# Kernel optimization log

Measured on AMD Instinct MI355X. Metric: run time of the kernel, lower is better.

## Reference

```python
import jax, jax.numpy as jnp
import numpy as np

NUM_IMAGE_PATCHES = 4096
HIDDEN = 1536
NUM_HEADS = 12
HEAD_DIM = HIDDEN // NUM_HEADS  # 128
MLP_HIDDEN = 4 * HIDDEN  # 6144
TXT_LEN = 256
L_X = TXT_LEN + NUM_IMAGE_PATCHES  # 4352
NUM_CONCEPTS = 20
L_C = NUM_CONCEPTS + NUM_IMAGE_PATCHES  # 4116


def setup_inputs() -> dict:
    key = jax.random.key(0)
    ks = jax.random.split(key, 10)
    B = 1
    f = lambda k, s, sc=1.0: jax.random.normal(k, s, dtype=jnp.float32) * sc
    return {
        "x": f(ks[0], (B, L_X, HIDDEN)),
        "concepts": f(ks[1], (B, NUM_CONCEPTS, HIDDEN)),
        "vec": f(ks[2], (B, HIDDEN)),
        "pe": f(ks[3], (1, 1, L_X, HEAD_DIM // 2, 2, 2)),
        "concept_pe": f(ks[4], (1, 1, L_C, HEAD_DIM // 2, 2, 2)),
        # linear1: hidden -> 3*hidden + mlp_hidden (torch Linear: y = x @ W.T + b)
        "w1": f(ks[5], (3 * HIDDEN + MLP_HIDDEN, HIDDEN), 0.02),
        "b1": jnp.zeros((3 * HIDDEN + MLP_HIDDEN,), jnp.float32),
        # linear2: hidden + mlp_hidden -> hidden
        "w2": f(ks[6], (HIDDEN, HIDDEN + MLP_HIDDEN), 0.02),
        "b2": jnp.zeros((HIDDEN,), jnp.float32),
        # QKNorm learned RMSNorm scales (per head_dim)
        "q_scale": jnp.ones((HEAD_DIM,), jnp.float32),
        "k_scale": jnp.ones((HEAD_DIM,), jnp.float32),
        # Modulation(double=False): silu(vec) -> 3*hidden (shift, scale, gate)
        "mod_w": f(ks[7], (3 * HIDDEN, HIDDEN), 0.02),
        "mod_b": jnp.zeros((3 * HIDDEN,), jnp.float32),
    }


def _layernorm(x):  # elementwise_affine=False, eps=1e-6
    mu = x.mean(-1, keepdims=True)
    var = ((x - mu) ** 2).mean(-1, keepdims=True)
    return (x - mu) * jax.lax.rsqrt(var + 1e-6)


def _rmsnorm(x, scale):  # FLUX RMSNorm with learned scale
    return x * jax.lax.rsqrt((x * x).mean(-1, keepdims=True) + 1e-6) * scale


def _apply_rope(t, pe):
    # t: [B,H,L,D]; pe: [1,1,L,D/2,2,2]
    ts = t.reshape(*t.shape[:-1], -1, 1, 2)  # [B,H,L,D/2,1,2]
    out = pe[..., 0] * ts[..., 0] + pe[..., 1] * ts[..., 1]  # [B,H,L,D/2,2]
    return out.reshape(t.shape)


def _attention(q, k, v, pe):
    q = _apply_rope(q, pe)
    k = _apply_rope(k, pe)
    scale = jnp.asarray(1.0 / np.sqrt(q.shape[-1]), q.dtype)
    logits = jnp.einsum("bhqd,bhkd->bhqk", q, k) * scale
    a = jax.nn.softmax(logits, axis=-1)
    o = jnp.einsum("bhqk,bhkd->bhqd", a, v)
    B, H, L, D = o.shape
    return o.transpose(0, 2, 1, 3).reshape(B, L, H * D)  # B L (H D)


def reference(x, concepts, vec, pe, concept_pe, w1, b1, w2, b2,
              q_scale, k_scale, mod_w, mod_b):
    H = HIDDEN
    # Modulation: lin(silu(vec))[:, None].chunk(3) -> shift, scale, gate
    m = jax.nn.silu(vec) @ mod_w.T + mod_b
    shift, scale, gate = [t[:, None, :] for t in jnp.split(m, 3, axis=-1)]

    def block(inp, pe_in):
        xm = (1.0 + scale) * _layernorm(inp) + shift
        h = xm @ w1.T + b1
        qkv, mlp = h[..., : 3 * H], h[..., 3 * H:]
        B, L = inp.shape[0], inp.shape[1]
        # 'B L (K H D) -> K B H L D'
        qkv = qkv.reshape(B, L, 3, NUM_HEADS, HEAD_DIM).transpose(2, 0, 3, 1, 4)
        q, k, v = qkv[0], qkv[1], qkv[2]
        q = _rmsnorm(q, q_scale)
        k = _rmsnorm(k, k_scale)
        attn = _attention(q, k, v, pe_in)
        return jnp.concatenate([attn, jax.nn.gelu(mlp, approximate=True)], axis=2) @ w2.T + b2

    output = block(x, pe)

    img = x[:, -NUM_IMAGE_PATCHES:]
    img_concept_x = jnp.concatenate([concepts, img], axis=1)
    output_img_concept = block(img_concept_x, concept_pe)
    concept_output = output_img_concept[:, :-NUM_IMAGE_PATCHES]

    return (x + gate * output, concepts + gate * concept_output)
```

## Files before the change

### kernel.cpp

```cpp
#include <hip/hip_runtime.h>
#include <cstdint>
#include <cstddef>

typedef float        f32x4  __attribute__((ext_vector_type(4)));
typedef __bf16       bf16x8 __attribute__((ext_vector_type(8)));
typedef unsigned int u32x4  __attribute__((ext_vector_type(4)));
typedef unsigned int u32x2  __attribute__((ext_vector_type(2)));

static constexpr int HID   = 1536;
static constexpr int NHEAD = 12;
static constexpr int HD    = 128;
static constexpr int NQKV  = 10752;
static constexpr int CATK  = 7680;
static constexpr int LX    = 4352;
static constexpr int LC2   = 4116;
static constexpr int NCON  = 20;

static constexpr float QSCL = 0.08838834764831845f * 1.4426950408889634f;

static constexpr size_t OFF_MVEC = 0;
static constexpr size_t OFF_W1B  = 18432;
static constexpr size_t OFF_W2B  = OFF_W1B  + 33030144ull;
static constexpr size_t OFF_XM1  = OFF_W2B  + 23592960ull;
static constexpr size_t OFF_QH1  = OFF_XM1;
static constexpr size_t OFF_QKV1 = OFF_XM1  + 13369344ull;
static constexpr size_t OFF_KH1  = OFF_QKV1 + 26738688ull;
static constexpr size_t OFF_VH1  = OFF_KH1  + 13369344ull;
static constexpr size_t OFF_CAT1 = OFF_VH1  + 13369344ull;
static constexpr size_t OFF_XM2  = OFF_CAT1;
static constexpr size_t OFF_QKV2 = OFF_XM2  + 196608ull;
static constexpr size_t OFF_VH2S = OFF_QKV2 + 196608ull;
static constexpr size_t OFF_QH2  = OFF_VH2S + 98304ull;
static constexpr size_t OFF_KH2  = OFF_QH2  + 196608ull;
static constexpr size_t OFF_CAT2 = OFF_KH2  + 12644352ull;

__device__ __forceinline__ void gload_lds16(const void* g, void* l)
{
  __builtin_amdgcn_global_load_lds(
      (const __attribute__((address_space(1))) unsigned int*)g,
      (__attribute__((address_space(3))) unsigned int*)l, 16, 0, 0);
}


__global__ __launch_bounds__(256) void f2b_kernel(const float* __restrict__ in,
                                                  __bf16* __restrict__ out, int n4)
{
  int i = blockIdx.x * 256 + threadIdx.x;
  if (i >= n4) return;
  f32x4 v = *((const f32x4*)in + i);
  union { __bf16 h[4]; u32x2 u; } cv;
  cv.h[0] = (__bf16)v[0]; cv.h[1] = (__bf16)v[1];
  cv.h[2] = (__bf16)v[2]; cv.h[3] = (__bf16)v[3];
  *((u32x2*)out + i) = cv.u;
}

__global__ __launch_bounds__(256) void mod_kernel(const float* __restrict__ vec,
                                                  const float* __restrict__ mod_w,
                                                  const float* __restrict__ mod_b,
                                                  float* __restrict__ m)
{
  int o = blockIdx.x * 4 + (threadIdx.x >> 6);
  int lane = threadIdx.x & 63;
  float s = 0.0f;
  for (int k = lane; k < HID; k += 64) {
    float v = vec[k];
    float sv = v / (1.0f + expf(-v));
    s += sv * mod_w[(size_t)o * HID + k];
  }
  #pragma unroll
  for (int msk = 32; msk; msk >>= 1) s += __shfl_xor(s, msk);
  if (lane == 0) m[o] = s + mod_b[o];
}

__device__ __forceinline__ float block_sum256(float v, float* red)
{
  #pragma unroll
  for (int msk = 32; msk; msk >>= 1) v += __shfl_xor(v, msk);
  int w = threadIdx.x >> 6;
  if ((threadIdx.x & 63) == 0) red[w] = v;
  __syncthreads();
  float s = red[0] + red[1] + red[2] + red[3];
  __syncthreads();
  return s;
}

__global__ __launch_bounds__(256) void ln_mod_kernel(const float* __restrict__ x,
                                                     const float* __restrict__ mvec,
                                                     __bf16* __restrict__ out)
{
  __shared__ float red[4];
  size_t row = blockIdx.x;
  const float* xr = x + row * HID;
  float v[6]; float s = 0.0f;
  #pragma unroll
  for (int i = 0; i < 6; i++) { v[i] = xr[threadIdx.x + i * 256]; s += v[i]; }
  float mu = block_sum256(s, red) * (1.0f / HID);
  float s2 = 0.0f;
  #pragma unroll
  for (int i = 0; i < 6; i++) { float d = v[i] - mu; s2 += d * d; }
  float var = block_sum256(s2, red) * (1.0f / HID);
  float rinv = rsqrtf(var + 1e-6f);
  #pragma unroll
  for (int i = 0; i < 6; i++) {
    int h = threadIdx.x + i * 256;
    float xm = (v[i] - mu) * rinv;
    xm = (1.0f + mvec[HID + h]) * xm + mvec[h];
    out[row * HID + h] = (__bf16)xm;
  }
}

template<int MODE>
__global__ __launch_bounds__(256) void gemm_bt(const __bf16* __restrict__ A,
                                               const __bf16* __restrict__ B,
                                               int M, int K,
                                               const float* __restrict__ bias,
                                               __bf16* __restrict__ qkv_out,
                                               __bf16* __restrict__ cat_out,
                                               __bf16* __restrict__ vh_out, int vkeys,
                                               const float* __restrict__ res,
                                               const float* __restrict__ gate,
                                               float* __restrict__ out)
{
  const int tid = threadIdx.x;
  const int lane = tid & 63, wave = tid >> 6;
  const int quad = lane >> 4, l16 = lane & 15;
  const int m0 = blockIdx.y * 128, n0 = blockIdx.x * 128;
  const int wm = (wave & 1) * 64, wn = (wave >> 1) * 64;

  __shared__ __bf16 As[128][64];
  __shared__ __bf16 Bs[128][64];

  const f32x4 fzero = {0.0f, 0.0f, 0.0f, 0.0f};
  f32x4 acc[4][4];
  #pragma unroll
  for (int i = 0; i < 4; i++)
    #pragma unroll
    for (int j = 0; j < 4; j++) acc[i][j] = fzero;

  const int srow = lane >> 3;
  const int scol = (lane & 7) * 8;
  const int rbase = wave * 32 + srow;
  const __bf16* Ab = A + (size_t)(m0 + rbase) * K + scol;
  const __bf16* Bb = B + (size_t)(n0 + rbase) * K + scol;

  for (int k0 = 0; k0 < K; k0 += 64) {
    __syncthreads();
    #pragma unroll
    for (int j = 0; j < 4; j++) {
      gload_lds16(Ab + (size_t)(j * 8) * K + k0, &As[wave * 32 + j * 8][0]);
      gload_lds16(Bb + (size_t)(j * 8) * K + k0, &Bs[wave * 32 + j * 8][0]);
    }
    __syncthreads();
    #pragma unroll
    for (int kk = 0; kk < 64; kk += 32) {
      bf16x8 af[4], bfr[4];
      #pragma unroll
      for (int i = 0; i < 4; i++) af[i]  = *(const bf16x8*)&As[wm + i * 16 + l16][kk + quad * 8];
      #pragma unroll
      for (int j = 0; j < 4; j++) bfr[j] = *(const bf16x8*)&Bs[wn + j * 16 + l16][kk + quad * 8];
      #pragma unroll
      for (int i = 0; i < 4; i++)
        #pragma unroll
        for (int j = 0; j < 4; j++)
          acc[i][j] = __builtin_amdgcn_mfma_f32_16x16x32_bf16(af[i], bfr[j], acc[i][j], 0, 0, 0);
    }
  }

  #pragma unroll
  for (int i = 0; i < 4; i++) {
    #pragma unroll
    for (int r = 0; r < 4; r++) {
      int gm = m0 + wm + i * 16 + quad * 4 + r;
      if (gm >= M) continue;
      #pragma unroll
      for (int j = 0; j < 4; j++) {
        int gn = n0 + wn + j * 16 + l16;
        float v = acc[i][j][r] + bias[gn];
        if constexpr (MODE == 0) {
          if (gn < 3072) {
            qkv_out[(size_t)gm * 3072 + gn] = (__bf16)v;
          } else if (gn < 4608) {
            vh_out[(size_t)(gn - 3072) * vkeys + gm] = (__bf16)v;
          } else {
            float g = 0.5f * v * (1.0f + tanhf(0.7978845608028654f * (v + 0.044715f * v * v * v)));
            cat_out[(size_t)gm * CATK + (gn - 3072)] = (__bf16)g;
          }
        } else {
          out[(size_t)gm * HID + gn] = res[(size_t)gm * HID + gn] + gate[gn] * v;
        }
      }
    }
  }
}

__global__ __launch_bounds__(256) void qk_prep(const __bf16* __restrict__ src0, int rows0,
                                               const __bf16* __restrict__ src1, int off1,
                                               int total_rows, int q_rows,
                                               const float* __restrict__ pe,
                                               const float* __restrict__ qscale,
                                               const float* __restrict__ kscale,
                                               __bf16* __restrict__ qh, int q_stride,
                                               __bf16* __restrict__ kh, int k_stride)
{
  int wid = blockIdx.x * 4 + (threadIdx.x >> 6);
  int lane = threadIdx.x & 63;
  int r = wid / NHEAD, h = wid - (wid / NHEAD) * NHEAD;
  if (r >= total_rows) return;
  const __bf16* src = (r < rows0) ? (src0 + (size_t)r * 3072)
                                  : (src1 + (size_t)(r + off1) * 3072);
  const float* pep = pe + ((size_t)r * 64 + lane) * 4;
  float e00 = pep[0], e01 = pep[1], e10 = pep[2], e11 = pep[3];

  {
    const __bf16* p = src + HID + h * HD + 2 * lane;
    float a = (float)p[0], b = (float)p[1];
    float ss = a * a + b * b;
    #pragma unroll
    for (int msk = 32; msk; msk >>= 1) ss += __shfl_xor(ss, msk);
    float rinv = rsqrtf(ss * (1.0f / HD) + 1e-6f);
    a *= rinv * kscale[2 * lane]; b *= rinv * kscale[2 * lane + 1];
    float ra = e00 * a + e01 * b, rb = e10 * a + e11 * b;
    __bf16* o = kh + ((size_t)h * k_stride + r) * HD + 2 * lane;
    o[0] = (__bf16)ra; o[1] = (__bf16)rb;
  }
  if (r < q_rows) {
    const __bf16* p = src + h * HD + 2 * lane;
    float a = (float)p[0], b = (float)p[1];
    float ss = a * a + b * b;
    #pragma unroll
    for (int msk = 32; msk; msk >>= 1) ss += __shfl_xor(ss, msk);
    float rinv = rsqrtf(ss * (1.0f / HD) + 1e-6f);
    a *= rinv * qscale[2 * lane]; b *= rinv * qscale[2 * lane + 1];
    float ra = (e00 * a + e01 * b) * QSCL, rb = (e10 * a + e11 * b) * QSCL;
    __bf16* o = qh + ((size_t)h * q_stride + r) * HD + 2 * lane;
    o[0] = (__bf16)ra; o[1] = (__bf16)rb;
  }
}

template<int GEN>
__global__ __launch_bounds__(512, 4) void attn_kernel(const __bf16* __restrict__ qh,
                                                      const __bf16* __restrict__ kh,
                                                      const __bf16* __restrict__ vA, int vA_stride,
                                                      const __bf16* __restrict__ vB, int vB_stride,
                                                      int v_boff, int v_split,
                                                      int Lq, int Lk, int q_stride, int k_stride,
                                                      int nqt,
                                                      __bf16* __restrict__ cat_out)
{
  const int tid = threadIdx.x, lane = tid & 63, wave = tid >> 6;
  const int quad = lane >> 4, l16 = lane & 15;
  const int qsub = wave >> 1, kg = wave & 1;

  int bid = blockIdx.x;
  if constexpr (GEN == 0) {
    int nb = gridDim.x;
    if ((nb & 7) == 0) {
      int per = nb >> 3;
      bid = (bid & 7) * per + (bid >> 3);
    }
  }
  const int head = bid / nqt, qt = bid - head * nqt;
  const int q0 = qt * 64 + qsub * 16;

  __shared__ __align__(16) unsigned char lds_raw[46080];
  __bf16 (*Ks)[136]     = (__bf16(*)[136])(lds_raw);
  __bf16 (*Vt)[72]      = (__bf16(*)[72])(lds_raw + 17408);
  __bf16 (*Ps)[16][40]  = (__bf16(*)[16][40])(lds_raw + 35840);
  float*  Of            = (float*)lds_raw;
  float (*Lml)[16][2]   = (float(*)[16][2])(lds_raw + 35840);

  const f32x4 fzero = {0.0f, 0.0f, 0.0f, 0.0f};
  const u32x4 uzero = {0, 0, 0, 0};

  bf16x8 ones;
  #pragma unroll
  for (int e = 0; e < 8; e++) ones[e] = (__bf16)1.0f;

  bf16x8 qf[4];
  {
    int qrow = q0 + l16;
    if (GEN == 0 || qrow < Lq) {
      const __bf16* qp = qh + ((size_t)head * q_stride + qrow) * HD + quad * 8;
      #pragma unroll
      for (int c = 0; c < 4; c++) qf[c] = *(const bf16x8*)(qp + c * 32);
    } else {
      #pragma unroll
      for (int c = 0; c < 4; c++) qf[c] = __builtin_bit_cast(bf16x8, uzero);
    }
  }
  f32x4 o[8];
  #pragma unroll
  for (int d = 0; d < 8; d++) o[d] = fzero;
  f32x4 l_acc = fzero;
  float m_r[4] = {-1e30f, -1e30f, -1e30f, -1e30f};

  const int krowA = tid >> 4, kcolA = (tid & 15) * 8;
  const int vdimA = tid >> 3, vkcA  = tid & 7;

  const __bf16* khb = kh + (size_t)head * k_stride * HD;
  const __bf16* vaB = vA + (size_t)head * HD * vA_stride;
  const __bf16* vbB = vB + (size_t)head * HD * vB_stride + v_boff;

  auto vload = [&](int dim, int kb) -> u32x4 {
    if constexpr (GEN == 0) {
      return *(const u32x4*)(vbB + (size_t)dim * vB_stride + kb);
    } else {
      u32x4 vd = uzero;
      if (kb < Lk) {
        if (kb + 8 <= v_split) {
          vd = *(const u32x4*)(vaB + (size_t)dim * vA_stride + kb);
        } else if (kb >= v_split && kb + 8 <= Lk) {
          vd = *(const u32x4*)(vbB + (size_t)dim * vB_stride + kb);
        } else {
          __bf16* ve = (__bf16*)&vd;
          #pragma unroll
          for (int e = 0; e < 8; e++) {
            int key = kb + e;
            if (key < Lk)
              ve[e] = (key < v_split) ? vaB[(size_t)dim * vA_stride + key]
                                      : vbB[(size_t)dim * vB_stride + key];
          }
        }
      }
      return vd;
    }
  };
  auto kload = [&](int kr, int col) -> u32x4 {
    if constexpr (GEN == 0) {
      return *(const u32x4*)(khb + (size_t)kr * HD + col);
    } else {
      return (kr < Lk) ? *(const u32x4*)(khb + (size_t)kr * HD + col) : uzero;
    }
  };

  u32x4 pk0, pk1, pv0, pv1;
  pk0 = kload(krowA, kcolA);
  pk1 = kload(krowA + 32, kcolA);
  pv0 = vload(vdimA, vkcA * 8);
  pv1 = vload(vdimA + 64, vkcA * 8);

  const int nkt = (Lk + 63) >> 6;
  for (int t = 0; t < nkt; ++t) {
    const int kt0 = t * 64;
    __syncthreads();
    *(u32x4*)&Ks[krowA][kcolA]      = pk0;
    *(u32x4*)&Ks[krowA + 32][kcolA] = pk1;
    *(u32x4*)&Vt[vdimA][vkcA * 8]      = pv0;
    *(u32x4*)&Vt[vdimA + 64][vkcA * 8] = pv1;
    if (t + 1 < nkt) {
      const int nt0 = kt0 + 64;
      pk0 = kload(nt0 + krowA, kcolA);
      pk1 = kload(nt0 + krowA + 32, kcolA);
      pv0 = vload(vdimA, nt0 + vkcA * 8);
      pv1 = vload(vdimA + 64, nt0 + vkcA * 8);
    }
    __syncthreads();

    f32x4 s[2];
    __builtin_amdgcn_s_setprio(1);
    #pragma unroll
    for (int nt = 0; nt < 2; nt++) {
      s[nt] = fzero;
      #pragma unroll
      for (int c = 0; c < 4; c++) {
        bf16x8 b = *(const bf16x8*)&Ks[kg * 32 + nt * 16 + l16][c * 32 + quad * 8];
        s[nt] = __builtin_amdgcn_mfma_f32_16x16x32_bf16(qf[c], b, s[nt], 0, 0, 0);
      }
      if constexpr (GEN != 0) {
        int kidx = kt0 + kg * 32 + nt * 16 + l16;
        if (kidx >= Lk) { s[nt][0] = -1e30f; s[nt][1] = -1e30f; s[nt][2] = -1e30f; s[nt][3] = -1e30f; }
      }
    }
    __builtin_amdgcn_s_setprio(0);

    float rm[4];
    #pragma unroll
    for (int r = 0; r < 4; r++) {
      float tmax = fmaxf(s[0][r], s[1][r]);
      tmax = fmaxf(tmax, __shfl_xor(tmax, 1));
      tmax = fmaxf(tmax, __shfl_xor(tmax, 2));
      tmax = fmaxf(tmax, __shfl_xor(tmax, 4));
      tmax = fmaxf(tmax, __shfl_xor(tmax, 8));
      rm[r] = tmax;
    }
    bool grow = (rm[0] > m_r[0] + 8.0f) || (rm[1] > m_r[1] + 8.0f)
             || (rm[2] > m_r[2] + 8.0f) || (rm[3] > m_r[3] + 8.0f);
    if (__any(grow)) {
      #pragma unroll
      for (int r = 0; r < 4; r++) {
        float mn = fmaxf(m_r[r], rm[r]);
        float alpha = exp2f(m_r[r] - mn);
        m_r[r] = mn;
        l_acc[r] *= alpha;
        #pragma unroll
        for (int d = 0; d < 8; d++) o[d][r] *= alpha;
      }
    }
    #pragma unroll
    for (int r = 0; r < 4; r++) {
      int prow = quad * 4 + r;
      Ps[wave][prow][l16]      = (__bf16)exp2f(s[0][r] - m_r[r]);
      Ps[wave][prow][16 + l16] = (__bf16)exp2f(s[1][r] - m_r[r]);
    }

    bf16x8 pf = *(const bf16x8*)&Ps[wave][l16][quad * 8];
    __builtin_amdgcn_s_setprio(1);
    l_acc = __builtin_amdgcn_mfma_f32_16x16x32_bf16(pf, ones, l_acc, 0, 0, 0);
    #pragma unroll
    for (int dt = 0; dt < 8; dt++) {
      bf16x8 bv = *(const bf16x8*)&Vt[dt * 16 + l16][kg * 32 + quad * 8];
      o[dt] = __builtin_amdgcn_mfma_f32_16x16x32_bf16(pf, bv, o[dt], 0, 0, 0);
    }
    __builtin_amdgcn_s_setprio(0);
  }

  __syncthreads();
  if (l16 == 0) {
    #pragma unroll
    for (int r = 0; r < 4; r++) {
      Lml[wave][quad * 4 + r][0] = m_r[r];
      Lml[wave][quad * 4 + r][1] = l_acc[r];
    }
  }
  __syncthreads();
  float a_self[4], inv_den[4];
  {
    const int other = wave ^ 1;
    #pragma unroll
    for (int r = 0; r < 4; r++) {
      int row = quad * 4 + r;
      float m_o = Lml[other][row][0], l_o = Lml[other][row][1];
      float M = fmaxf(m_r[r], m_o);
      float as = exp2f(m_r[r] - M), ao = exp2f(m_o - M);
      a_self[r] = as;
      inv_den[r] = 1.0f / (as * l_acc[r] + ao * l_o);
    }
  }
  if (kg == 0) {
    #pragma unroll
    for (int d = 0; d < 8; d++)
      #pragma unroll
      for (int r = 0; r < 4; r++)
        Of[(size_t)(qsub * 16 + quad * 4 + r) * 132 + d * 16 + l16] = o[d][r] * a_self[r];
  }
  __syncthreads();
  if (kg == 1) {
    #pragma unroll
    for (int r = 0; r < 4; r++) {
      int qrow = q0 + quad * 4 + r;
      if (qrow >= Lq) continue;
      #pragma unroll
      for (int d = 0; d < 8; d++) {
        float v = Of[(size_t)(qsub * 16 + quad * 4 + r) * 132 + d * 16 + l16]
                  + o[d][r] * a_self[r];
        cat_out[(size_t)qrow * CATK + head * HD + d * 16 + l16] = (__bf16)(v * inv_den[r]);
      }
    }
  }
}

extern "C" void kernel_launch(void* const* d_in, const int* in_sizes, int n_in,
                              void* d_out, int out_size, void* d_ws, size_t ws_size,
                              hipStream_t stream)
{
  const float* x   = (const float*)d_in[0];
  const float* con = (const float*)d_in[1];
  const float* vec = (const float*)d_in[2];
  const float* pe  = (const float*)d_in[3];
  const float* cpe = (const float*)d_in[4];
  const float* w1  = (const float*)d_in[5];
  const float* b1  = (const float*)d_in[6];
  const float* w2  = (const float*)d_in[7];
  const float* b2  = (const float*)d_in[8];
  const float* qsc = (const float*)d_in[9];
  const float* ksc = (const float*)d_in[10];
  const float* mw  = (const float*)d_in[11];
  const float* mb  = (const float*)d_in[12];
  float* out = (float*)d_out;

  char* ws = (char*)d_ws;
  float*  mvec = (float*)(ws + OFF_MVEC);
  __bf16* w1b  = (__bf16*)(ws + OFF_W1B);
  __bf16* w2b  = (__bf16*)(ws + OFF_W2B);
  __bf16* xm1  = (__bf16*)(ws + OFF_XM1);
  __bf16* qh1  = (__bf16*)(ws + OFF_QH1);
  __bf16* qkv1 = (__bf16*)(ws + OFF_QKV1);
  __bf16* kh1  = (__bf16*)(ws + OFF_KH1);
  __bf16* vh1  = (__bf16*)(ws + OFF_VH1);
  __bf16* cat1 = (__bf16*)(ws + OFF_CAT1);
  __bf16* xm2  = (__bf16*)(ws + OFF_XM2);
  __bf16* qkv2 = (__bf16*)(ws + OFF_QKV2);
  __bf16* vh2s = (__bf16*)(ws + OFF_VH2S);
  __bf16* qh2  = (__bf16*)(ws + OFF_QH2);
  __bf16* kh2  = (__bf16*)(ws + OFF_KH2);
  __bf16* cat2 = (__bf16*)(ws + OFF_CAT2);

  f2b_kernel<<<16128, 256, 0, stream>>>(w1, w1b, (NQKV * HID) / 4);
  f2b_kernel<<<11520, 256, 0, stream>>>(w2, w2b, (HID * CATK) / 4);
  mod_kernel<<<1152, 256, 0, stream>>>(vec, mw, mb, mvec);

  ln_mod_kernel<<<LX, 256, 0, stream>>>(x, mvec, xm1);
  gemm_bt<0><<<dim3(NQKV / 128, LX / 128), 256, 0, stream>>>(
      xm1, w1b, LX, HID, b1, qkv1, cat1, vh1, LX, nullptr, nullptr, nullptr);
  qk_prep<<<(LX * NHEAD) / 4, 256, 0, stream>>>(
      qkv1, LX, qkv1, 0, LX, LX, pe, qsc, ksc, qh1, LX, kh1, LX);
  attn_kernel<0><<<NHEAD * (LX / 64), 512, 0, stream>>>(
      qh1, kh1, vh1, LX, vh1, LX, 0, 0, LX, LX, LX, LX, LX / 64, cat1);
  gemm_bt<1><<<dim3(HID / 128, LX / 128), 256, 0, stream>>>(
      cat1, w2b, LX, CATK, b2, nullptr, nullptr, nullptr, 0, x, mvec + 3072, out);

  ln_mod_kernel<<<NCON, 256, 0, stream>>>(con, mvec, xm2);
  gemm_bt<0><<<dim3(NQKV / 128, 1), 256, 0, stream>>>(
      xm2, w1b, NCON, HID, b1, qkv2, cat2, vh2s, 32, nullptr, nullptr, nullptr);
  qk_prep<<<(LC2 * NHEAD + 3) / 4, 256, 0, stream>>>(
      qkv2, NCON, qkv1, 236, LC2, NCON, cpe, qsc, ksc, qh2, 64, kh2, LC2);
  attn_kernel<1><<<NHEAD, 512, 0, stream>>>(
      qh2, kh2, vh2s, 32, vh1, LX, 236, NCON, NCON, LC2, 64, LC2, 1, cat2);
  gemm_bt<1><<<dim3(HID / 128, 1), 256, 0, stream>>>(
      cat2, w2b, NCON, CATK, b2, nullptr, nullptr, nullptr, 0, con, mvec + 3072,
      out + (size_t)LX * HID);
}
```

Measured before the change: 1.402 ms.

## Add 256x256-tile 8-wave GEMM with interleaved LDS staging for large GEMMs

Adds a new GEMM kernel that uses 256x256 output tiles, 512 threads and double-buffered LDS filled by direct global-to-LDS loads. Prefetches are interleaved between MFMA phases, with s_setprio raising priority around the MFMA blocks. It replaces the 128x128 GEMM for both large linear layers, to raise data reuse per tile and overlap loads with compute. The larger tiles mean fewer blocks (42x17 and 6x17), so wave quantization and lower occupancy from 64KB of LDS and the big accumulator are possible risks, especially for the N=1536 second GEMM.

Measured after the change: 1.449 ms. 3.3% more time.

```diff
diff --git a/kernel.cpp b/kernel.cpp
--- a/kernel.cpp
+++ b/kernel.cpp
@@ -41,6 +41,11 @@
       (__attribute__((address_space(3))) unsigned int*)l, 16, 0, 0);
 }
 
+__device__ __forceinline__ void wg_barrier()
+{
+  asm volatile("s_waitcnt lgkmcnt(0)\n\ts_barrier" ::: "memory");
+}
+
 
 __global__ __launch_bounds__(256) void f2b_kernel(const float* __restrict__ in,
                                                   __bf16* __restrict__ out, int n4)
@@ -106,6 +111,165 @@
     float xm = (v[i] - mu) * rinv;
     xm = (1.0f + mvec[HID + h]) * xm + mvec[h];
     out[row * HID + h] = (__bf16)xm;
+  }
+}
+
+template<int MODE>
+__global__ __launch_bounds__(512, 2) void gemm256(const __bf16* __restrict__ A,
+                                                  const __bf16* __restrict__ B,
+                                                  int M, int K,
+                                                  const float* __restrict__ bias,
+                                                  __bf16* __restrict__ qkv_out,
+                                                  __bf16* __restrict__ cat_out,
+                                                  __bf16* __restrict__ vh_out, int vkeys,
+                                                  const float* __restrict__ res,
+                                                  const float* __restrict__ gate,
+                                                  float* __restrict__ out)
+{
+  const int tid = threadIdx.x;
+  const int lane = tid & 63, wave = tid >> 6;
+  const int quad = lane >> 4, l16 = lane & 15;
+  const int wmh = wave >> 2;
+  const int wnq = wave & 3;
+  const int m0 = blockIdx.y * 256, n0 = blockIdx.x * 256;
+  const int swz = (l16 & 4) ? 16 : 0;
+
+  __shared__ __bf16 As[2][256][64];
+  __shared__ __bf16 Bs[2][256][64];
+
+  const f32x4 fzero = {0.0f, 0.0f, 0.0f, 0.0f};
+  f32x4 acc[8][4];
+  #pragma unroll
+  for (int i = 0; i < 8; i++)
+    #pragma unroll
+    for (int j = 0; j < 4; j++) acc[i][j] = fzero;
+
+  const int srow = lane >> 3;
+  const int scol = ((lane & 7) * 8) ^ ((lane & 32) ? 16 : 0);
+  const __bf16* Ag = A + (size_t)(m0 + wave * 32 + srow) * K + scol;
+  const __bf16* Bg = B + (size_t)(n0 + wave * 32 + srow) * K + scol;
+
+  auto stageA = [&](int buf, int k) {
+    #pragma unroll
+    for (int j = 0; j < 4; j++)
+      gload_lds16(Ag + (size_t)(j * 8) * K + k, &As[buf][wave * 32 + j * 8][0]);
+  };
+  auto stageB = [&](int buf, int k) {
+    #pragma unroll
+    for (int j = 0; j < 4; j++)
+      gload_lds16(Bg + (size_t)(j * 8) * K + k, &Bs[buf][wave * 32 + j * 8][0]);
+  };
+
+  const int NT = K >> 6;
+  stageB(0, 0);  stageA(0, 0);
+  stageB(1, 64); stageA(1, 64);
+  asm volatile("s_waitcnt vmcnt(8)" ::: "memory");
+  wg_barrier();
+
+  for (int t = 0; t < NT; ++t) {
+    const int b = t & 1;
+    const int kn = (t + 2) << 6;
+    bf16x8 aM[4][2], bN0[2][2], bN1[2][2];
+
+    #pragma unroll
+    for (int f = 0; f < 4; f++)
+      #pragma unroll
+      for (int kk = 0; kk < 2; kk++)
+        aM[f][kk] = *(const bf16x8*)&As[b][wmh * 128 + f * 16 + l16][(kk * 32 + quad * 8) ^ swz];
+    #pragma unroll
+    for (int g = 0; g < 2; g++)
+      #pragma unroll
+      for (int kk = 0; kk < 2; kk++)
+        bN0[g][kk] = *(const bf16x8*)&Bs[b][wnq * 64 + g * 16 + l16][(kk * 32 + quad * 8) ^ swz];
+    wg_barrier();
+    __builtin_amdgcn_s_setprio(1);
+    #pragma unroll
+    for (int f = 0; f < 4; f++)
+      #pragma unroll
+      for (int g = 0; g < 2; g++)
+        #pragma unroll
+        for (int kk = 0; kk < 2; kk++)
+          acc[f][g] = __builtin_amdgcn_mfma_f32_16x16x32_bf16(aM[f][kk], bN0[g][kk], acc[f][g], 0, 0, 0);
+    __builtin_amdgcn_s_setprio(0);
+    wg_barrier();
+
+    #pragma unroll
+    for (int g = 0; g < 2; g++)
+      #pragma unroll
+      for (int kk = 0; kk < 2; kk++)
+        bN1[g][kk] = *(const bf16x8*)&Bs[b][wnq * 64 + 32 + g * 16 + l16][(kk * 32 + quad * 8) ^ swz];
+    wg_barrier();
+    __builtin_amdgcn_s_setprio(1);
+    #pragma unroll
+    for (int f = 0; f < 4; f++)
+      #pragma unroll
+      for (int g = 0; g < 2; g++)
+        #pragma unroll
+        for (int kk = 0; kk < 2; kk++)
+          acc[f][2 + g] = __builtin_amdgcn_mfma_f32_16x16x32_bf16(aM[f][kk], bN1[g][kk], acc[f][2 + g], 0, 0, 0);
+    __builtin_amdgcn_s_setprio(0);
+    wg_barrier();
+
+    #pragma unroll
+    for (int f = 0; f < 4; f++)
+      #pragma unroll
+      for (int kk = 0; kk < 2; kk++)
+        aM[f][kk] = *(const bf16x8*)&As[b][wmh * 128 + 64 + f * 16 + l16][(kk * 32 + quad * 8) ^ swz];
+    if (t + 2 < NT) stageB(b, kn);
+    wg_barrier();
+    __builtin_amdgcn_s_setprio(1);
+    #pragma unroll
+    for (int f = 0; f < 4; f++)
+      #pragma unroll
+      for (int g = 0; g < 2; g++)
+        #pragma unroll
+        for (int kk = 0; kk < 2; kk++)
+          acc[4 + f][2 + g] = __builtin_amdgcn_mfma_f32_16x16x32_bf16(aM[f][kk], bN1[g][kk], acc[4 + f][2 + g], 0, 0, 0);
+    __builtin_amdgcn_s_setprio(0);
+    wg_barrier();
+
+    if (t + 2 < NT) stageA(b, kn);
+    wg_barrier();
+    __builtin_amdgcn_s_setprio(1);
+    #pragma unroll
+    for (int f = 0; f < 4; f++)
+      #pragma unroll
+      for (int g = 0; g < 2; g++)
+        #pragma unroll
+        for (int kk = 0; kk < 2; kk++)
+          acc[4 + f][g] = __builtin_amdgcn_mfma_f32_16x16x32_bf16(aM[f][kk], bN0[g][kk], acc[4 + f][g], 0, 0, 0);
+    __builtin_amdgcn_s_setprio(0);
+    if (t + 1 < NT) {
+      if (t + 2 < NT) asm volatile("s_waitcnt vmcnt(8)" ::: "memory");
+      else            asm volatile("s_waitcnt vmcnt(0)" ::: "memory");
+    }
+    wg_barrier();
+  }
+
+  #pragma unroll
+  for (int mf = 0; mf < 8; mf++) {
+    #pragma unroll
+    for (int r = 0; r < 4; r++) {
+      int gm = m0 + wmh * 128 + mf * 16 + quad * 4 + r;
+      if (gm >= M) continue;
+      #pragma unroll
+      for (int nf = 0; nf < 4; nf++) {
+        int gn = n0 + wnq * 64 + nf * 16 + l16;
+        float v = acc[mf][nf][r] + bias[gn];
+        if constexpr (MODE == 0) {
+          if (gn < 3072) {
+            qkv_out[(size_t)gm * 3072 + gn] = (__bf16)v;
+          } else if (gn < 4608) {
+            vh_out[(size_t)(gn - 3072) * vkeys + gm] = (__bf16)v;
+          } else {
+            float g = 0.5f * v * (1.0f + tanhf(0.7978845608028654f * (v + 0.044715f * v * v * v)));
+            cat_out[(size_t)gm * CATK + (gn - 3072)] = (__bf16)g;
+          }
+        } else {
+          out[(size_t)gm * HID + gn] = res[(size_t)gm * HID + gn] + gate[gn] * v;
+        }
+      }
+    }
   }
 }
 
@@ -500,13 +664,13 @@
   mod_kernel<<<1152, 256, 0, stream>>>(vec, mw, mb, mvec);
 
   ln_mod_kernel<<<LX, 256, 0, stream>>>(x, mvec, xm1);
-  gemm_bt<0><<<dim3(NQKV / 128, LX / 128), 256, 0, stream>>>(
+  gemm256<0><<<dim3(NQKV / 256, LX / 256), 512, 0, stream>>>(
       xm1, w1b, LX, HID, b1, qkv1, cat1, vh1, LX, nullptr, nullptr, nullptr);
   qk_prep<<<(LX * NHEAD) / 4, 256, 0, stream>>>(
       qkv1, LX, qkv1, 0, LX, LX, pe, qsc, ksc, qh1, LX, kh1, LX);
   attn_kernel<0><<<NHEAD * (LX / 64), 512, 0, stream>>>(
       qh1, kh1, vh1, LX, vh1, LX, 0, 0, LX, LX, LX, LX, LX / 64, cat1);
-  gemm_bt<1><<<dim3(HID / 128, LX / 128), 256, 0, stream>>>(
+  gemm256<1><<<dim3(HID / 256, LX / 256), 512, 0, stream>>>(
       cat1, w2b, LX, CATK, b2, nullptr, nullptr, nullptr, 0, x, mvec + 3072, out);
 
   ln_mod_kernel<<<NCON, 256, 0, stream>>>(con, mvec, xm2);
```
